# Kernel tuning notes

Measured on AMD Instinct MI355X. Metric: run time of the kernel, lower is better.

Reference implementation:

```python
import jax, jax.numpy as jnp
import numpy as np

C, H, W = 3, 224, 224
P = 14  # patches per row
PS = H // P  # 16
PATCH_DIM = C * PS * PS  # 768
HIDDEN = 768


def patchify(images):
    # images: [n, c, h, w] -> [n, P*P, c*PS*PS], flatten order (c, ph, pw)
    n = images.shape[0]
    x = images.reshape(n, C, P, PS, P, PS)
    x = x.transpose(0, 2, 4, 1, 3, 5)  # [n, Pi, Pj, c, ps, ps]
    return x.reshape(n, P * P, PATCH_DIM)


def setup_inputs() -> dict:
    key = jax.random.key(0)
    k1, k2, k3 = jax.random.split(key, 3)
    images = jax.random.normal(k1, (128, C, H, W), dtype=jnp.float32)
    # nn.Linear(patch_embedding_dim, hidden_dim): weight [out, in], bias [out]
    bound = 1.0 / np.sqrt(PATCH_DIM)
    W_lin = jax.random.uniform(k2, (HIDDEN, PATCH_DIM), minval=-bound, maxval=bound, dtype=jnp.float32)
    b_lin = jax.random.uniform(k3, (HIDDEN,), minval=-bound, maxval=bound, dtype=jnp.float32)
    cls_token = jnp.ones((1, HIDDEN), dtype=jnp.float32)
    return {"images": images, "W_lin": W_lin, "b_lin": b_lin, "cls_token": cls_token}


def reference(images, W_lin, b_lin, cls_token):
    patches = patchify(images)                        # [n, 196, 768]
    hidden = jnp.einsum('npd,hd->nph', patches, W_lin) + b_lin  # [n, 196, H]
    n = images.shape[0]
    cls = jnp.broadcast_to(cls_token[None], (n, 1, HIDDEN))
    return jnp.concatenate([cls, hidden], axis=1)     # [n, 197, H]
```

## Files before the change

kernel.cpp:

```cpp
#include <hip/hip_runtime.h>
#include <cstdint>


#define PGRID 14
#define PSZ   16
#define CHN   3
#define IMGW  224
#define KDIM  768
#define NDIM  768
#define NPATCH 196
#define K32   24

typedef short bf16x8 __attribute__((ext_vector_type(8)));
typedef short short8v __attribute__((ext_vector_type(8)));
typedef float f32x4  __attribute__((ext_vector_type(4)));

__device__ __forceinline__ short bf16rne(float f) {
    uint32_t u = __builtin_bit_cast(uint32_t, f);
    u += 0x7FFFu + ((u >> 16) & 1u);
    return (short)(u >> 16);
}

__device__ __forceinline__ short8v cvt8(float4 v0, float4 v1) {
    short8v s;
    s[0] = bf16rne(v0.x); s[1] = bf16rne(v0.y); s[2] = bf16rne(v0.z); s[3] = bf16rne(v0.w);
    s[4] = bf16rne(v1.x); s[5] = bf16rne(v1.y); s[6] = bf16rne(v1.z); s[7] = bf16rne(v1.w);
    return s;
}

__global__ __launch_bounds__(256) void prep_patch(
    const float* __restrict__ img, short* __restrict__ A, int M)
{
    int t = blockIdx.x * 256 + threadIdx.x;
    if (t >= M * 96) return;
    int m  = t / 96;
    int k8 = t - m * 96;
    int k  = k8 * 8;
    int c  = k >> 8;
    int ph = (k >> 4) & 15;
    int pw = k & 15;
    int im = m / NPATCH;
    int p  = m - im * NPATCH;
    int Pi = p / PGRID;
    int Pj = p - Pi * PGRID;
    const float* src = img + (((long)(im * CHN + c) * IMGW + Pi * PSZ + ph) * IMGW + Pj * PSZ + pw);
    float4 v0 = *(const float4*)src;
    float4 v1 = *(const float4*)(src + 4);
    int m16  = m >> 4;
    int k32  = k8 >> 2;
    int quad = k8 & 3;
    int lane = (m & 15) | (quad << 4);
    *(short8v*)(A + (((long)m16 * K32 + k32) << 9) + lane * 8) = cvt8(v0, v1);
}

__global__ __launch_bounds__(256) void prep_small(
    const float* __restrict__ Wl, const float* __restrict__ cls,
    short* __restrict__ Wb, float* __restrict__ out, int n_img)
{
    int t = blockIdx.x * 256 + threadIdx.x;
    const int WCH = KDIM * NDIM / 8;
    if (t < WCH) {
        int n  = t / 96;
        int k8 = t - n * 96;
        float4 v0 = *(const float4*)(Wl + (long)n * KDIM + k8 * 8);
        float4 v1 = *(const float4*)(Wl + (long)n * KDIM + k8 * 8 + 4);
        int n16  = n >> 4;
        int k32  = k8 >> 2;
        int quad = k8 & 3;
        int lane = (n & 15) | (quad << 4);
        *(short8v*)(Wb + (((long)n16 * K32 + k32) << 9) + lane * 8) = cvt8(v0, v1);
    } else {
        int u = t - WCH;
        if (u < n_img * 96) {
            int im = u / 96;
            int k8 = u - im * 96;
            float4 v0 = *(const float4*)(cls + k8 * 8);
            float4 v1 = *(const float4*)(cls + k8 * 8 + 4);
            float* dst = out + (long)im * 197 * NDIM + k8 * 8;
            *(float4*)dst = v0;
            *(float4*)(dst + 4) = v1;
        }
    }
}

__global__ __launch_bounds__(256, 2) void vit_gemm4(
    const short* __restrict__ A, const short* __restrict__ B,
    const float* __restrict__ bias, float* __restrict__ out,
    int M, int mgroups)
{
    const int bid = blockIdx.x;
    const int xcd = bid & 7;
    const int s   = bid >> 3;
    const int gq  = s / 6;
    const int j   = s - gq * 6;
    const int g   = gq * 8 + xcd;
    if (g >= mgroups) return;
    const int m0 = g * 256;
    const int n0 = j * 128;

    const int tid  = threadIdx.x;
    const int wave = tid >> 6;
    const int lane = tid & 63;
    const int wq   = lane >> 4;
    const int lr   = lane & 15;

    const short* Ab = A + (((long)((m0 >> 4) + wave * 4) * K32) << 9) + lane * 8;
    const short* Bb = B + (((long)(n0 >> 4) * K32) << 9) + lane * 8;
    const long fstride = (long)K32 << 9;

    f32x4 acc[4][8] = {};
    bf16x8 a0[4], b0[8], a1[4], b1[8];

#define LDA(dst, kk) { _Pragma("unroll") for (int i = 0; i < 4; ++i) \
        dst[i] = *(const bf16x8*)(Ab + i * fstride + ((kk) << 9)); }
#define LDB(dst, kk) { _Pragma("unroll") for (int i = 0; i < 8; ++i) \
        dst[i] = *(const bf16x8*)(Bb + i * fstride + ((kk) << 9)); }
#define MM(aa, bb) { _Pragma("unroll") for (int i = 0; i < 4; ++i) \
        _Pragma("unroll") for (int q = 0; q < 8; ++q) \
        acc[i][q] = __builtin_amdgcn_mfma_f32_16x16x32_bf16(aa[i], bb[q], acc[i][q], 0, 0, 0); }

    LDA(a0, 0); LDB(b0, 0);
    for (int k = 0; k < K32; k += 2) {
        LDA(a1, k + 1); LDB(b1, k + 1);
        MM(a0, b0);
        if (k + 2 < K32) { LDA(a0, k + 2); LDB(b0, k + 2); }
        MM(a1, b1);
    }
#undef LDA
#undef LDB
#undef MM

    float bv[8];
    #pragma unroll
    for (int q = 0; q < 8; ++q) bv[q] = bias[n0 + q * 16 + lr];

    const int mw = m0 + wave * 64;
    #pragma unroll
    for (int i = 0; i < 4; ++i) {
        #pragma unroll
        for (int r = 0; r < 4; ++r) {
            int gm = mw + i * 16 + wq * 4 + r;
            if (gm < M) {
                int im = gm / NPATCH;
                int p  = gm - im * NPATCH;
                float* orow = out + ((long)im * 197 + 1 + p) * NDIM + n0 + lr;
                #pragma unroll
                for (int q = 0; q < 8; ++q)
                    orow[q * 16] = acc[i][q][r] + bv[q];
            }
        }
    }
}

#define LDSTR 40
__global__ __launch_bounds__(256) void vit_gemm_fb(
    const float* __restrict__ img, const float* __restrict__ Wl,
    const float* __restrict__ bias, float* __restrict__ out, int n_img)
{
    const int M = n_img * NPATCH;
    __shared__ short As[128 * LDSTR];
    __shared__ short Bs[128 * LDSTR];
    const int tid = threadIdx.x;
    const int m0 = blockIdx.y * 128;
    const int n0 = blockIdx.x * 128;
    const int col4  = tid & 7;
    const int rbase = tid >> 3;
    long arow[4];
    for (int rr = 0; rr < 4; ++rr) {
        int m = m0 + rbase + rr * 32;
        int mm = (m < M) ? m : (M - 1);
        int im = mm / NPATCH;
        int p  = mm % NPATCH;
        int Pi = p / PGRID;
        int Pj = p % PGRID;
        arow[rr] = ((long)(im * CHN) * IMGW + Pi * PSZ) * IMGW + Pj * PSZ;
    }
    const int lane = tid & 63;
    const int wave = tid >> 6;
    const int wm = (wave & 1) * 64;
    const int wn = (wave >> 1) * 64;
    const int wq = lane >> 4;
    const int lr = lane & 15;
    f32x4 acc[4][4] = {};
    for (int k0 = 0; k0 < KDIM; k0 += 32) {
        {
            int k  = k0 + col4 * 4;
            int c  = k >> 8;
            int ph = (k >> 4) & 15;
            int pw = k & 15;
            long koff = (long)(c * IMGW + ph) * IMGW + pw;
            #pragma unroll
            for (int rr = 0; rr < 4; ++rr) {
                const float4 v = *(const float4*)(img + arow[rr] + koff);
                int row = rbase + rr * 32;
                short4 s;
                s.x = bf16rne(v.x); s.y = bf16rne(v.y);
                s.z = bf16rne(v.z); s.w = bf16rne(v.w);
                *(short4*)(&As[row * LDSTR + col4 * 4]) = s;
            }
        }
        {
            int k = k0 + col4 * 4;
            #pragma unroll
            for (int rr = 0; rr < 4; ++rr) {
                int nrow = rbase + rr * 32;
                const float4 v = *(const float4*)(Wl + (long)(n0 + nrow) * KDIM + k);
                short4 s;
                s.x = bf16rne(v.x); s.y = bf16rne(v.y);
                s.z = bf16rne(v.z); s.w = bf16rne(v.w);
                *(short4*)(&Bs[nrow * LDSTR + col4 * 4]) = s;
            }
        }
        __syncthreads();
        bf16x8 a[4], b[4];
        #pragma unroll
        for (int i = 0; i < 4; ++i)
            a[i] = *(const bf16x8*)(&As[(wm + i * 16 + lr) * LDSTR + wq * 8]);
        #pragma unroll
        for (int i = 0; i < 4; ++i)
            b[i] = *(const bf16x8*)(&Bs[(wn + i * 16 + lr) * LDSTR + wq * 8]);
        #pragma unroll
        for (int i = 0; i < 4; ++i)
            #pragma unroll
            for (int j = 0; j < 4; ++j)
                acc[i][j] = __builtin_amdgcn_mfma_f32_16x16x32_bf16(a[i], b[j], acc[i][j], 0, 0, 0);
        __syncthreads();
    }
    float bv[4];
    #pragma unroll
    for (int j = 0; j < 4; ++j) bv[j] = bias[n0 + wn + j * 16 + lr];
    #pragma unroll
    for (int i = 0; i < 4; ++i) {
        #pragma unroll
        for (int r = 0; r < 4; ++r) {
            int gm = m0 + wm + i * 16 + wq * 4 + r;
            if (gm < M) {
                int im = gm / NPATCH;
                int p  = gm % NPATCH;
                long orow = ((long)im * 197 + 1 + p) * (long)NDIM;
                #pragma unroll
                for (int j = 0; j < 4; ++j)
                    out[orow + n0 + wn + j * 16 + lr] = acc[i][j][r] + bv[j];
            }
        }
    }
}

__global__ __launch_bounds__(256) void cls_fill(
    const float* __restrict__ cls, float* __restrict__ out, int n_img)
{
    int i = blockIdx.x * 256 + threadIdx.x;
    if (i < n_img * NDIM) {
        int im = i / NDIM;
        int n  = i - im * NDIM;
        out[(long)im * 197 * NDIM + n] = cls[n];
    }
}

extern "C" void kernel_launch(void* const* d_in, const int* in_sizes, int n_in,
                              void* d_out, int out_size, void* d_ws, size_t ws_size,
                              hipStream_t stream) {
    const float* img  = (const float*)d_in[0];
    const float* Wl   = (const float*)d_in[1];
    const float* bias = (const float*)d_in[2];
    const float* cls  = (const float*)d_in[3];
    float* out = (float*)d_out;

    int n_img = in_sizes[0] / (CHN * IMGW * IMGW);
    int M = n_img * NPATCH;
    int mgroups = (M + 255) / 256;
    long Mpad = (long)mgroups * 256;

    size_t need = (size_t)(Mpad * KDIM + (long)KDIM * NDIM) * sizeof(short);
    if (ws_size >= need) {
        short* A_ws = (short*)d_ws;
        short* Wb   = A_ws + Mpad * KDIM;

        prep_patch<<<(M * 96 + 255) / 256, 256, 0, stream>>>(img, A_ws, M);
        int small_total = KDIM * NDIM / 8 + n_img * 96;
        prep_small<<<(small_total + 255) / 256, 256, 0, stream>>>(Wl, cls, Wb, out, n_img);

        int gpad = (mgroups + 7) & ~7;
        int nblocks = gpad * 6;
        vit_gemm4<<<nblocks, 256, 0, stream>>>(A_ws, Wb, bias, out, M, mgroups);
    } else {
        int mb = (M + 127) / 128;
        dim3 grid(NDIM / 128, mb);
        vit_gemm_fb<<<grid, 256, 0, stream>>>(img, Wl, bias, out, n_img);
        int cls_elems = n_img * NDIM;
        cls_fill<<<(cls_elems + 255) / 256, 256, 0, stream>>>(cls, out, n_img);
    }
}
```

Baseline: 190.5 us.

## Shrink GEMM tile to 128x128 with 2x2 wave grid and remap prep threads

The GEMM block tile shrinks from 256x128 to 128x128. The four waves are now arranged 2x2, so each wave computes a 64x64 tile, cutting accumulators in half, and launch bounds rise to 3 blocks per CU for more occupancy and twice as many blocks. Separately, the prep kernels remap thread indices so that 16 consecutive threads handle 16 consecutive rows at the same k-chunk. This makes the packed-layout writes contiguous, at the cost of strided reads from the images and weights. Smaller tiles also reduce reuse of each loaded fragment, which raises total operand traffic from global memory.

```diff
diff --git a/kernel.cpp b/kernel.cpp
--- a/kernel.cpp
+++ b/kernel.cpp
@@ -33,8 +33,11 @@
 {
     int t = blockIdx.x * 256 + threadIdx.x;
     if (t >= M * 96) return;
-    int m  = t / 96;
-    int k8 = t - m * 96;
+    int mlow = t & 15;
+    int r    = t >> 4;
+    int G    = r / 96;
+    int k8   = r - G * 96;
+    int m    = G * 16 + mlow;
     int k  = k8 * 8;
     int c  = k >> 8;
     int ph = (k >> 4) & 15;
@@ -46,11 +49,10 @@
     const float* src = img + (((long)(im * CHN + c) * IMGW + Pi * PSZ + ph) * IMGW + Pj * PSZ + pw);
     float4 v0 = *(const float4*)src;
     float4 v1 = *(const float4*)(src + 4);
-    int m16  = m >> 4;
     int k32  = k8 >> 2;
     int quad = k8 & 3;
-    int lane = (m & 15) | (quad << 4);
-    *(short8v*)(A + (((long)m16 * K32 + k32) << 9) + lane * 8) = cvt8(v0, v1);
+    int lane = mlow | (quad << 4);
+    *(short8v*)(A + (((long)G * K32 + k32) << 9) + lane * 8) = cvt8(v0, v1);
 }
 
 __global__ __launch_bounds__(256) void prep_small(
@@ -60,15 +62,17 @@
     int t = blockIdx.x * 256 + threadIdx.x;
     const int WCH = KDIM * NDIM / 8;
     if (t < WCH) {
-        int n  = t / 96;
-        int k8 = t - n * 96;
+        int nlow = t & 15;
+        int r    = t >> 4;
+        int G    = r / 96;
+        int k8   = r - G * 96;
+        int n    = G * 16 + nlow;
         float4 v0 = *(const float4*)(Wl + (long)n * KDIM + k8 * 8);
         float4 v1 = *(const float4*)(Wl + (long)n * KDIM + k8 * 8 + 4);
-        int n16  = n >> 4;
         int k32  = k8 >> 2;
         int quad = k8 & 3;
-        int lane = (n & 15) | (quad << 4);
-        *(short8v*)(Wb + (((long)n16 * K32 + k32) << 9) + lane * 8) = cvt8(v0, v1);
+        int lane = nlow | (quad << 4);
+        *(short8v*)(Wb + (((long)G * K32 + k32) << 9) + lane * 8) = cvt8(v0, v1);
     } else {
         int u = t - WCH;
         if (u < n_img * 96) {
@@ -83,7 +87,7 @@
     }
 }
 
-__global__ __launch_bounds__(256, 2) void vit_gemm4(
+__global__ __launch_bounds__(256, 3) void vit_gemm5(
     const short* __restrict__ A, const short* __restrict__ B,
     const float* __restrict__ bias, float* __restrict__ out,
     int M, int mgroups)
@@ -95,7 +99,7 @@
     const int j   = s - gq * 6;
     const int g   = gq * 8 + xcd;
     if (g >= mgroups) return;
-    const int m0 = g * 256;
+    const int m0 = g * 128;
     const int n0 = j * 128;
 
     const int tid  = threadIdx.x;
@@ -103,38 +107,38 @@
     const int lane = tid & 63;
     const int wq   = lane >> 4;
     const int lr   = lane & 15;
-
-    const short* Ab = A + (((long)((m0 >> 4) + wave * 4) * K32) << 9) + lane * 8;
-    const short* Bb = B + (((long)(n0 >> 4) * K32) << 9) + lane * 8;
+    const int wm   = (wave & 1) * 64;
+    const int wn   = (wave >> 1) * 64;
+
+    const short* Ab = A + (((long)((m0 + wm) >> 4) * K32) << 9) + lane * 8;
+    const short* Bb = B + (((long)((n0 + wn) >> 4) * K32) << 9) + lane * 8;
     const long fstride = (long)K32 << 9;
 
-    f32x4 acc[4][8] = {};
-    bf16x8 a0[4], b0[8], a1[4], b1[8];
-
-#define LDA(dst, kk) { _Pragma("unroll") for (int i = 0; i < 4; ++i) \
-        dst[i] = *(const bf16x8*)(Ab + i * fstride + ((kk) << 9)); }
-#define LDB(dst, kk) { _Pragma("unroll") for (int i = 0; i < 8; ++i) \
-        dst[i] = *(const bf16x8*)(Bb + i * fstride + ((kk) << 9)); }
+    f32x4 acc[4][4] = {};
+    bf16x8 a0[4], b0[4], a1[4], b1[4];
+
+#define LD(da, db, kk) { _Pragma("unroll") for (int i = 0; i < 4; ++i) { \
+        da[i] = *(const bf16x8*)(Ab + i * fstride + ((kk) << 9)); \
+        db[i] = *(const bf16x8*)(Bb + i * fstride + ((kk) << 9)); } }
 #define MM(aa, bb) { _Pragma("unroll") for (int i = 0; i < 4; ++i) \
-        _Pragma("unroll") for (int q = 0; q < 8; ++q) \
+        _Pragma("unroll") for (int q = 0; q < 4; ++q) \
         acc[i][q] = __builtin_amdgcn_mfma_f32_16x16x32_bf16(aa[i], bb[q], acc[i][q], 0, 0, 0); }
 
-    LDA(a0, 0); LDB(b0, 0);
+    LD(a0, b0, 0);
     for (int k = 0; k < K32; k += 2) {
-        LDA(a1, k + 1); LDB(b1, k + 1);
+        LD(a1, b1, k + 1);
         MM(a0, b0);
-        if (k + 2 < K32) { LDA(a0, k + 2); LDB(b0, k + 2); }
+        if (k + 2 < K32) LD(a0, b0, k + 2);
         MM(a1, b1);
     }
-#undef LDA
-#undef LDB
+#undef LD
 #undef MM
 
-    float bv[8];
-    #pragma unroll
-    for (int q = 0; q < 8; ++q) bv[q] = bias[n0 + q * 16 + lr];
-
-    const int mw = m0 + wave * 64;
+    float bv[4];
+    #pragma unroll
+    for (int q = 0; q < 4; ++q) bv[q] = bias[n0 + wn + q * 16 + lr];
+
+    const int mw = m0 + wm;
     #pragma unroll
     for (int i = 0; i < 4; ++i) {
         #pragma unroll
@@ -143,9 +147,9 @@
             if (gm < M) {
                 int im = gm / NPATCH;
                 int p  = gm - im * NPATCH;
-                float* orow = out + ((long)im * 197 + 1 + p) * NDIM + n0 + lr;
+                float* orow = out + ((long)im * 197 + 1 + p) * NDIM + n0 + wn + lr;
                 #pragma unroll
-                for (int q = 0; q < 8; ++q)
+                for (int q = 0; q < 4; ++q)
                     orow[q * 16] = acc[i][q][r] + bv[q];
             }
         }
@@ -268,8 +272,8 @@
 
     int n_img = in_sizes[0] / (CHN * IMGW * IMGW);
     int M = n_img * NPATCH;
-    int mgroups = (M + 255) / 256;
-    long Mpad = (long)mgroups * 256;
+    int mgroups = (M + 127) / 128;
+    long Mpad = (long)mgroups * 128;
 
     size_t need = (size_t)(Mpad * KDIM + (long)KDIM * NDIM) * sizeof(short);
     if (ws_size >= need) {
@@ -282,7 +286,7 @@
 
         int gpad = (mgroups + 7) & ~7;
         int nblocks = gpad * 6;
-        vit_gemm4<<<nblocks, 256, 0, stream>>>(A_ws, Wb, bias, out, M, mgroups);
+        vit_gemm5<<<nblocks, 256, 0, stream>>>(A_ws, Wb, bias, out, M, mgroups);
     } else {
         int mb = (M + 127) / 128;
         dim3 grid(NDIM / 128, mb);
```

Result: no change. 193.3 us (+1.5%).
